# Kernel tuning notes

Hardware: AMD Instinct MI355X
Metric: run time of the kernel (lower is better)

## Reference

```python
import jax, jax.numpy as jnp
import numpy as np

DIM = 1024
EPS = 1e-5

def layer_norm(x, gamma, beta):
    mu = jnp.mean(x, axis=-1, keepdims=True)
    var = jnp.mean(jnp.square(x - mu), axis=-1, keepdims=True)
    return (x - mu) * jax.lax.rsqrt(var + EPS) * gamma + beta

def setup_inputs() -> dict:
    key = jax.random.key(0)
    k1, k2 = jax.random.split(key)
    B, Nv, Nt = 8, 4096, 4096
    visual_tokens = jax.random.normal(k1, (B, Nv, DIM), dtype=jnp.float32)
    text_tokens = jax.random.normal(k2, (B, Nt, DIM), dtype=jnp.float32)
    gamma_v = jnp.ones((DIM,), dtype=jnp.float32)
    beta_v = jnp.zeros((DIM,), dtype=jnp.float32)
    gamma_t = jnp.ones((DIM,), dtype=jnp.float32)
    beta_t = jnp.zeros((DIM,), dtype=jnp.float32)
    return {"visual_tokens": visual_tokens, "text_tokens": text_tokens,
            "gamma_v": gamma_v, "beta_v": beta_v,
            "gamma_t": gamma_t, "beta_t": beta_t}

def reference(visual_tokens, text_tokens, gamma_v, beta_v, gamma_t, beta_t):
    # Dual LayerNorm
    V = layer_norm(visual_tokens, gamma_v, beta_v)   # [B, Nv, D]
    T = layer_norm(text_tokens, gamma_t, beta_t)     # [B, Nt, D]
    scale = jnp.sqrt(jnp.asarray(DIM, dtype=V.dtype))  # note: sqrt(dim), per source
    scores = jnp.einsum('bvd,btd->bvt', V, T) / scale  # [B, Nv, Nt]
    attn = jax.nn.softmax(scores, axis=-1)
    out = jnp.einsum('bvt,btd->bvd', attn, T)          # [B, Nv, D]
    return out
```

## Files before the change

kernel.cpp:

```cpp
#include <hip/hip_runtime.h>
#include <hip/hip_bf16.h>
#include <stdint.h>

#define DIMD 1024
#define NSEQ 4096
#define BATCH 8
#define LN_EPS 1e-5f

typedef __attribute__((ext_vector_type(8))) short bf16x8;
typedef __attribute__((ext_vector_type(4))) float f32x4;
typedef __attribute__((ext_vector_type(4))) unsigned int u32x4;

__device__ __forceinline__ ushort f2bf(float f) {
  union { __hip_bfloat16 h; ushort u; } cv;
  cv.h = __float2bfloat16(f);
  return cv.u;
}

__device__ __forceinline__ float fexp2(float x) {
  return exp2f(x);
}

__device__ __forceinline__ void gload16(const void* g, void* l) {
  __builtin_amdgcn_global_load_lds(
      (const __attribute__((address_space(1))) uint32_t*)g,
      (__attribute__((address_space(3))) uint32_t*)l, 16, 0, 0);
}

#define MIDBAR()   asm volatile("s_barrier" ::: "memory")
#define ENDBAR()   asm volatile("s_waitcnt lgkmcnt(0)\n\ts_barrier" ::: "memory")
#define ENDBARV4() asm volatile("s_waitcnt vmcnt(4) lgkmcnt(0)\n\ts_barrier" ::: "memory")
#define ENDBARV0() asm volatile("s_waitcnt vmcnt(0) lgkmcnt(0)\n\ts_barrier" ::: "memory")

__device__ __forceinline__ int swz64(int byte) {
  return byte ^ (((byte >> 7) & 3) << 4);
}

__global__ __launch_bounds__(256) void ln_bf16_kernel(
    const float* __restrict__ x, const float* __restrict__ gamma,
    const float* __restrict__ beta, ushort* __restrict__ y, float scale)
{
  const int lane = threadIdx.x & 63;
  const int wv   = threadIdx.x >> 6;
  const size_t row = (size_t)blockIdx.x * 4 + wv;
  const float* xr = x + row * DIMD;

  float4 v[4];
#pragma unroll
  for (int c = 0; c < 4; ++c)
    v[c] = *(const float4*)(xr + c * 256 + lane * 4);

  float s = 0.f;
#pragma unroll
  for (int c = 0; c < 4; ++c) s += v[c].x + v[c].y + v[c].z + v[c].w;
#pragma unroll
  for (int m = 32; m >= 1; m >>= 1) s += __shfl_xor(s, m, 64);
  const float mean = s * (1.0f / DIMD);

  float vs = 0.f;
#pragma unroll
  for (int c = 0; c < 4; ++c) {
    float a0 = v[c].x - mean, a1 = v[c].y - mean;
    float a2 = v[c].z - mean, a3 = v[c].w - mean;
    vs += a0 * a0 + a1 * a1 + a2 * a2 + a3 * a3;
  }
#pragma unroll
  for (int m = 32; m >= 1; m >>= 1) vs += __shfl_xor(vs, m, 64);
  const float rstd = rsqrtf(vs * (1.0f / DIMD) + LN_EPS);

  ushort* yr = y + row * DIMD;
#pragma unroll
  for (int c = 0; c < 4; ++c) {
    const int d = c * 256 + lane * 4;
    float4 g  = *(const float4*)(gamma + d);
    float4 bb = *(const float4*)(beta + d);
    ushort4 o;
    o.x = f2bf(((v[c].x - mean) * rstd * g.x + bb.x) * scale);
    o.y = f2bf(((v[c].y - mean) * rstd * g.y + bb.y) * scale);
    o.z = f2bf(((v[c].z - mean) * rstd * g.z + bb.z) * scale);
    o.w = f2bf(((v[c].w - mean) * rstd * g.w + bb.w) * scale);
    *(ushort4*)(yr + d) = o;
  }
}

__global__ __launch_bounds__(256) void transpose_kernel(
    const ushort* __restrict__ src, ushort* __restrict__ dst)
{
  __shared__ ushort tile[64][72];
  const int t   = threadIdx.x;
  const int bid = blockIdx.x;
  const int b   = bid >> 10;
  const int rem = bid & 1023;
  const int n0  = (rem >> 4) << 6;
  const int d0  = (rem & 15) << 6;
  const ushort* sb = src + ((size_t)b * NSEQ) * DIMD;
  ushort* db       = dst + ((size_t)b * DIMD) * NSEQ;

#pragma unroll
  for (int k = 0; k < 2; ++k) {
    int c = t + 256 * k;
    int r = c >> 3, scol = (c & 7) * 8;
    *(uint4*)&tile[r][scol] =
        *(const uint4*)(sb + (size_t)(n0 + r) * DIMD + d0 + scol);
  }
  __syncthreads();
#pragma unroll
  for (int k = 0; k < 2; ++k) {
    int c = t + 256 * k;
    int dr = c >> 3, ns = (c & 7) * 8;
    union { ushort u[8]; uint4 q; } tv;
#pragma unroll
    for (int i = 0; i < 8; ++i) tv.u[i] = tile[ns + i][dr];
    *(uint4*)(db + (size_t)(d0 + dr) * NSEQ + n0 + ns) = tv.q;
  }
}

__device__ __forceinline__ void stage_chunk(const ushort* __restrict__ g,
                                            int ld, char* l, int tid) {
  const int o0 = tid * 16;
  const int o1 = o0 + 8192;
  const int s0 = swz64(o0);
  const int s1 = swz64(o1);
  gload16(g + (size_t)(s0 >> 6) * ld + ((s0 & 63) >> 1), l + o0);
  gload16(g + (size_t)(s1 >> 6) * ld + ((s1 & 63) >> 1), l + o1);
}

__device__ __forceinline__ void stage_lin(const ushort* __restrict__ g,
                                          char* l, int tid) {
  gload16(g + tid * 8,        l + tid * 16);
  gload16(g + 4096 + tid * 8, l + tid * 16 + 8192);
}

__device__ __forceinline__ bf16x8 ldsw_read(const char* base, int row, int lg) {
  return *(const bf16x8*)(base + swz64(row * 64 + lg * 16));
}

__device__ __forceinline__ void read_af(const char* Ac, int wm, int mh,
                                        int l15, int lg, bf16x8 (&af)[4]) {
#pragma unroll
  for (int m = 0; m < 4; ++m)
    af[m] = ldsw_read(Ac, wm * 128 + (mh * 4 + m) * 16 + l15, lg);
}
__device__ __forceinline__ void read_bf(const char* Bc, int wn,
                                        int l15, int lg, bf16x8 (&bf)[4]) {
#pragma unroll
  for (int n = 0; n < 4; ++n)
    bf[n] = ldsw_read(Bc, wn * 64 + n * 16 + l15, lg);
}

#define MFMA16(BASE)                                                          \
  do {                                                                        \
    MIDBAR();                                                                 \
    __builtin_amdgcn_s_setprio(1);                                            \
    _Pragma("unroll")                                                         \
    for (int m = 0; m < 4; ++m)                                               \
      _Pragma("unroll")                                                       \
      for (int n = 0; n < 4; ++n)                                             \
        acc[(BASE) + m][n] = __builtin_amdgcn_mfma_f32_16x16x32_bf16(         \
            af[m], bf[n], acc[(BASE) + m][n], 0, 0, 0);                       \
    __builtin_amdgcn_s_setprio(0);                                            \
  } while (0)

template <bool LINB>
__device__ __forceinline__ void gemm_core_A(
    const ushort* __restrict__ Ab, const ushort* __restrict__ Bb,
    int lda, int ldb, int NT, char* smem, f32x4 (&acc)[8][4],
    int tid, int wm, int wn, int l15, int lg)
{
  stage_chunk(Ab, lda, smem + 0, tid);
  if (LINB) stage_lin(Bb, smem + 32768, tid);
  else      stage_chunk(Bb, ldb, smem + 32768, tid);
  stage_chunk(Ab + 32, lda, smem + 16384, tid);
  if (LINB) stage_lin(Bb + 8192, smem + 49152, tid);
  else      stage_chunk(Bb + 32, ldb, smem + 49152, tid);
  ENDBARV4();

  for (int kt = 0; kt < NT; ++kt) {
    char* cb = smem + (kt & 1) * 65536;
    char* nbuf = smem + (((kt & 1) ^ 1) * 65536);
    const ushort* An = Ab + (size_t)(kt + 1) * 64;
    const ushort* Bn = LINB ? (Bb + (size_t)(kt + 1) * 16384)
                            : (Bb + (size_t)(kt + 1) * 64);
    const bool pf = (kt + 1 < NT);
    bf16x8 af[4], bf[4];

    read_af(cb + 0, wm, 0, l15, lg, af);
    read_bf(cb + 32768, wn, l15, lg, bf);
    if (pf) stage_chunk(An, lda, nbuf + 0, tid);
    MFMA16(0);
    ENDBAR();

    read_af(cb + 0, wm, 1, l15, lg, af);
    if (pf) {
      if (LINB) stage_lin(Bn, nbuf + 32768, tid);
      else      stage_chunk(Bn, ldb, nbuf + 32768, tid);
    }
    MFMA16(4);
    if (pf) { ENDBARV4(); } else { ENDBARV0(); }

    read_af(cb + 16384, wm, 0, l15, lg, af);
    read_bf(cb + 49152, wn, l15, lg, bf);
    if (pf) stage_chunk(An + 32, lda, nbuf + 16384, tid);
    MFMA16(0);
    ENDBAR();

    read_af(cb + 16384, wm, 1, l15, lg, af);
    if (pf) {
      if (LINB) stage_lin(Bn + 8192, nbuf + 49152, tid);
      else      stage_chunk(Bn + 32, ldb, nbuf + 49152, tid);
    }
    MFMA16(4);
    if (pf) { ENDBARV4(); } else { ENDBAR(); }
  }
}

__global__ __launch_bounds__(512, 2) void gemm1_256(
    const ushort* __restrict__ Q, const ushort* __restrict__ K,
    ushort* __restrict__ S, float* __restrict__ Rsum,
    int b0, size_t s_stride)
{
  extern __shared__ char smem[];
  const int tid  = threadIdx.x;
  const int lane = tid & 63;
  const int wave = tid >> 6;
  const int wm = wave >> 2, wn = wave & 3;
  const int l15 = lane & 15, lg = lane >> 4;

  int by, bxx, bzc;
  if (gridDim.x == 8 * 64) {
    const int hw = blockIdx.x;
    bzc = hw & 7;
    const int inner = hw >> 3;
    bxx = inner & 3;
    by  = inner >> 2;
  } else {
    by = blockIdx.y; bxx = blockIdx.x; bzc = 0;
  }

  const int bz   = b0 + bzc;
  const int row0 = by * 256;
  const ushort* Qb = Q + (size_t)bz * NSEQ * DIMD + (size_t)row0 * DIMD;
  const ushort* Kb0 = K + (size_t)bz * NSEQ * DIMD;

  float vsum[4] = {0.f, 0.f, 0.f, 0.f};

#pragma unroll 1
  for (int st = 0; st < 4; ++st) {
    const int bx = bxx * 4 + st;
    const ushort* Kb = Kb0 + (size_t)(bx * 256) * DIMD;

    f32x4 acc[8][4];
#pragma unroll
    for (int m = 0; m < 8; ++m)
#pragma unroll
      for (int n = 0; n < 4; ++n) acc[m][n] = 0.0f;

    gemm_core_A<false>(Kb, Qb, DIMD, DIMD, DIMD / 64, smem, acc,
                       tid, wm, wn, l15, lg);

#pragma unroll
    for (int ti = 0; ti < 8; ++ti) {
      const int tl   = wm * 128 + ti * 16 + lg * 4;
      const int ktl  = tl >> 6;
      const int half = (tl >> 5) & 1;
      const int tcol = tl & 31;
      char* img = smem + (ktl * 2 + half) * 16384;
#pragma unroll
      for (int vi = 0; vi < 4; ++vi) {
        const int vrow = wn * 64 + vi * 16 + l15;
        float p0 = fexp2(acc[ti][vi][0]);
        float p1 = fexp2(acc[ti][vi][1]);
        float p2 = fexp2(acc[ti][vi][2]);
        float p3 = fexp2(acc[ti][vi][3]);
        vsum[vi] += (p0 + p1) + (p2 + p3);
        unsigned long long pk =
            (unsigned long long)f2bf(p0)        |
            ((unsigned long long)f2bf(p1) << 16) |
            ((unsigned long long)f2bf(p2) << 32) |
            ((unsigned long long)f2bf(p3) << 48);
        *(unsigned long long*)(img + swz64(vrow * 64 + tcol * 2)) = pk;
      }
    }
    __syncthreads();

    ushort* region = S + (size_t)bzc * s_stride
                   + (size_t)by * 1048576 + (size_t)bx * 65536;
#pragma unroll
    for (int j = 0; j < 16; ++j) {
      const int off = (j * 512 + tid) * 16;
      u32x4 vle = *(const u32x4*)(smem + off);
      __builtin_nontemporal_store(vle, (u32x4*)((char*)region + off));
    }
    __syncthreads();
  }

  float* Rs = Rsum + (size_t)bz * NSEQ;
#pragma unroll
  for (int vi = 0; vi < 4; ++vi) {
    float s = vsum[vi];
    s += __shfl_xor(s, 16, 64);
    s += __shfl_xor(s, 32, 64);
    if (lg == 0)
      atomicAdd(Rs + row0 + wn * 64 + vi * 16 + l15, s);
  }
}

__global__ __launch_bounds__(512, 2) void gemm2_256(
    const ushort* __restrict__ S, const ushort* __restrict__ Kt,
    const float* __restrict__ Rsum, float* __restrict__ Out,
    int b0, size_t s_stride)
{
  extern __shared__ char smem[];
  const int tid  = threadIdx.x;
  const int lane = tid & 63;
  const int wave = tid >> 6;
  const int wm = wave >> 2, wn = wave & 3;
  const int l15 = lane & 15, lg = lane >> 4;

  int bx, by, bzc;
  if (gridDim.z == BATCH) {
    const int hw = blockIdx.x + (blockIdx.y << 2) + (blockIdx.z << 6);
    bzc = hw & 7;
    const int inner = hw >> 3;
    bx = inner & 3; by = inner >> 2;
  } else {
    bx = blockIdx.x; by = blockIdx.y; bzc = 0;
  }

  const int bz   = b0 + bzc;
  const int row0 = by * 256;
  const int col0 = bx * 256;
  const ushort* Sbase = S + (size_t)bzc * s_stride + (size_t)by * 1048576;
  const ushort* Vtb = Kt + ((size_t)bz * DIMD + col0) * NSEQ;

  f32x4 acc[8][4];
#pragma unroll
  for (int m = 0; m < 8; ++m)
#pragma unroll
    for (int n = 0; n < 4; ++n) acc[m][n] = 0.0f;

  gemm_core_A<true>(Vtb, Sbase, NSEQ, 0, NSEQ / 64, smem, acc, tid, wm, wn, l15, lg);

  const float* Rs = Rsum + (size_t)bz * NSEQ;
  float* Ob = Out + (size_t)bz * NSEQ * DIMD;
  float inv[4];
#pragma unroll
  for (int vi = 0; vi < 4; ++vi)
    inv[vi] = 1.0f / Rs[row0 + wn * 64 + vi * 16 + l15];
#pragma unroll
  for (int di = 0; di < 8; ++di) {
#pragma unroll
    for (int vi = 0; vi < 4; ++vi) {
      const int v = row0 + wn * 64 + vi * 16 + l15;
      const int d = col0 + wm * 128 + di * 16 + lg * 4;
      f32x4 o = acc[di][vi] * inv[vi];
      *(f32x4*)(Ob + (size_t)v * DIMD + d) = o;
    }
  }
}

extern "C" void kernel_launch(void* const* d_in, const int* in_sizes, int n_in,
                              void* d_out, int out_size, void* d_ws, size_t ws_size,
                              hipStream_t stream) {
  const float* vis = (const float*)d_in[0];
  const float* txt = (const float*)d_in[1];
  const float* gv  = (const float*)d_in[2];
  const float* bv  = (const float*)d_in[3];
  const float* gt  = (const float*)d_in[4];
  const float* bt  = (const float*)d_in[5];
  float* out = (float*)d_out;

  const size_t tokens = (size_t)BATCH * NSEQ * DIMD;
  ushort* Qbf = (ushort*)d_ws;
  ushort* Kbf = Qbf + tokens;
  ushort* Ktb = Kbf + tokens;
  char*   wsb = (char*)d_ws;
  float*  Rsum = (float*)(wsb + 201326592);
  ushort* Sbuf = (ushort*)(wsb + 201457664);

  const size_t S_FULL = (size_t)BATCH * NSEQ * NSEQ * 2;
  const size_t NEED_FULL = 201457664 + S_FULL;

  ln_bf16_kernel<<<BATCH * NSEQ / 4, 256, 0, stream>>>(vis, gv, bv, Qbf,
                                                       0.045084219f);
  ln_bf16_kernel<<<BATCH * NSEQ / 4, 256, 0, stream>>>(txt, gt, bt, Kbf, 1.0f);
  transpose_kernel<<<BATCH * (NSEQ / 64) * (DIMD / 64), 256, 0, stream>>>(Kbf, Ktb);

  (void)hipFuncSetAttribute((const void*)gemm1_256,
                      hipFuncAttributeMaxDynamicSharedMemorySize, 131072);
  (void)hipFuncSetAttribute((const void*)gemm2_256,
                      hipFuncAttributeMaxDynamicSharedMemorySize, 131072);

  (void)hipMemsetAsync(Rsum, 0, (size_t)BATCH * NSEQ * sizeof(float), stream);

  if (ws_size >= NEED_FULL) {
    gemm1_256<<<dim3(8 * 64, 1, 1), 512, 131072, stream>>>(
        Qbf, Kbf, Sbuf, Rsum, 0, (size_t)NSEQ * NSEQ);
    gemm2_256<<<dim3(4, 16, BATCH), 512, 131072, stream>>>(
        Sbuf, Ktb, Rsum, out, 0, (size_t)NSEQ * NSEQ);
  } else {
    for (int b = 0; b < BATCH; ++b) {
      gemm1_256<<<dim3(4, 16, 1), 512, 131072, stream>>>(
          Qbf, Kbf, Sbuf, Rsum, b, 0);
      gemm2_256<<<dim3(4, 16, 1), 512, 131072, stream>>>(
          Sbuf, Ktb, Rsum, out, b, 0);
    }
  }
}
```

Baseline: 616.8 us.

## Flatten score GEMM into one pipelined K loop across column tiles, store P directly

Merges the four per-tile GEMM calls into a single 64-step double-buffered loop, so loads for the next column tile are prefetched while the current one finishes and no pipeline drain or refill happens between tiles. The exp2 and bf16 pack results are now written straight to global memory in the swizzled layout, replacing the LDS staging and the nontemporal copy-out along with its two block barriers. The costs are scattered 8-byte global stores in place of coalesced 16-byte nontemporal ones, and the softmax epilogue now runs inside the main loop.

```diff
diff --git a/kernel.cpp b/kernel.cpp
--- a/kernel.cpp
+++ b/kernel.cpp
@@ -9,7 +9,6 @@
 
 typedef __attribute__((ext_vector_type(8))) short bf16x8;
 typedef __attribute__((ext_vector_type(4))) float f32x4;
-typedef __attribute__((ext_vector_type(4))) unsigned int u32x4;
 
 __device__ __forceinline__ ushort f2bf(float f) {
   union { __hip_bfloat16 h; ushort u; } cv;
@@ -239,59 +238,87 @@
 
   const int bz   = b0 + bzc;
   const int row0 = by * 256;
-  const ushort* Qb = Q + (size_t)bz * NSEQ * DIMD + (size_t)row0 * DIMD;
-  const ushort* Kb0 = K + (size_t)bz * NSEQ * DIMD;
-
+  const ushort* Qb  = Q + (size_t)bz * NSEQ * DIMD + (size_t)row0 * DIMD;
+  const ushort* Kb0 = K + (size_t)bz * NSEQ * DIMD
+                    + (size_t)(bxx * 4) * 256 * DIMD;
+  char* Sreg = (char*)(S + (size_t)bzc * s_stride + (size_t)by * 1048576)
+             + (size_t)bxx * 4 * 131072;
+
+  f32x4 acc[8][4];
+#pragma unroll
+  for (int m = 0; m < 8; ++m)
+#pragma unroll
+    for (int n = 0; n < 4; ++n) acc[m][n] = 0.0f;
   float vsum[4] = {0.f, 0.f, 0.f, 0.f};
 
+  stage_chunk(Kb0,      DIMD, smem + 0,     tid);
+  stage_chunk(Qb,       DIMD, smem + 32768, tid);
+  stage_chunk(Kb0 + 32, DIMD, smem + 16384, tid);
+  stage_chunk(Qb + 32,  DIMD, smem + 49152, tid);
+  ENDBARV4();
+
 #pragma unroll 1
-  for (int st = 0; st < 4; ++st) {
-    const int bx = bxx * 4 + st;
-    const ushort* Kb = Kb0 + (size_t)(bx * 256) * DIMD;
-
-    f32x4 acc[8][4];
-#pragma unroll
-    for (int m = 0; m < 8; ++m)
-#pragma unroll
-      for (int n = 0; n < 4; ++n) acc[m][n] = 0.0f;
-
-    gemm_core_A<false>(Kb, Qb, DIMD, DIMD, DIMD / 64, smem, acc,
-                       tid, wm, wn, l15, lg);
-
-#pragma unroll
-    for (int ti = 0; ti < 8; ++ti) {
-      const int tl   = wm * 128 + ti * 16 + lg * 4;
-      const int ktl  = tl >> 6;
-      const int half = (tl >> 5) & 1;
-      const int tcol = tl & 31;
-      char* img = smem + (ktl * 2 + half) * 16384;
-#pragma unroll
-      for (int vi = 0; vi < 4; ++vi) {
-        const int vrow = wn * 64 + vi * 16 + l15;
-        float p0 = fexp2(acc[ti][vi][0]);
-        float p1 = fexp2(acc[ti][vi][1]);
-        float p2 = fexp2(acc[ti][vi][2]);
-        float p3 = fexp2(acc[ti][vi][3]);
-        vsum[vi] += (p0 + p1) + (p2 + p3);
-        unsigned long long pk =
-            (unsigned long long)f2bf(p0)        |
-            ((unsigned long long)f2bf(p1) << 16) |
-            ((unsigned long long)f2bf(p2) << 32) |
-            ((unsigned long long)f2bf(p3) << 48);
-        *(unsigned long long*)(img + swz64(vrow * 64 + tcol * 2)) = pk;
+  for (int kt = 0; kt < 64; ++kt) {
+    char* cb   = smem + (kt & 1) * 65536;
+    char* nbuf = smem + (((kt & 1) ^ 1) * 65536);
+    const int vn = kt + 1;
+    const bool pf = (vn < 64);
+    const ushort* An = Kb0 + (size_t)(vn >> 4) * 256 * DIMD + (vn & 15) * 64;
+    const ushort* Bn = Qb + (vn & 15) * 64;
+    bf16x8 af[4], bf[4];
+
+    read_af(cb + 0, wm, 0, l15, lg, af);
+    read_bf(cb + 32768, wn, l15, lg, bf);
+    if (pf) stage_chunk(An, DIMD, nbuf + 0, tid);
+    MFMA16(0);
+    ENDBAR();
+
+    read_af(cb + 0, wm, 1, l15, lg, af);
+    if (pf) stage_chunk(Bn, DIMD, nbuf + 32768, tid);
+    MFMA16(4);
+    if (pf) { ENDBARV4(); } else { ENDBARV0(); }
+
+    read_af(cb + 16384, wm, 0, l15, lg, af);
+    read_bf(cb + 49152, wn, l15, lg, bf);
+    if (pf) stage_chunk(An + 32, DIMD, nbuf + 16384, tid);
+    MFMA16(0);
+    ENDBAR();
+
+    read_af(cb + 16384, wm, 1, l15, lg, af);
+    if (pf) stage_chunk(Bn + 32, DIMD, nbuf + 49152, tid);
+    MFMA16(4);
+    if (pf) { ENDBARV4(); } else { ENDBAR(); }
+
+    if ((kt & 15) == 15) {
+      char* region = Sreg + (size_t)(kt >> 4) * 131072;
+#pragma unroll
+      for (int ti = 0; ti < 8; ++ti) {
+        const int tl   = wm * 128 + ti * 16 + lg * 4;
+        const int ktl  = tl >> 6;
+        const int half = (tl >> 5) & 1;
+        const int tcol = tl & 31;
+        char* img = region + (ktl * 2 + half) * 16384;
+#pragma unroll
+        for (int vi = 0; vi < 4; ++vi) {
+          const int vrow = wn * 64 + vi * 16 + l15;
+          float p0 = fexp2(acc[ti][vi][0]);
+          float p1 = fexp2(acc[ti][vi][1]);
+          float p2 = fexp2(acc[ti][vi][2]);
+          float p3 = fexp2(acc[ti][vi][3]);
+          vsum[vi] += (p0 + p1) + (p2 + p3);
+          unsigned long long pk =
+              (unsigned long long)f2bf(p0)        |
+              ((unsigned long long)f2bf(p1) << 16) |
+              ((unsigned long long)f2bf(p2) << 32) |
+              ((unsigned long long)f2bf(p3) << 48);
+          *(unsigned long long*)(img + swz64(vrow * 64 + tcol * 2)) = pk;
+        }
       }
+#pragma unroll
+      for (int m = 0; m < 8; ++m)
+#pragma unroll
+        for (int n = 0; n < 4; ++n) acc[m][n] = 0.0f;
     }
-    __syncthreads();
-
-    ushort* region = S + (size_t)bzc * s_stride
-                   + (size_t)by * 1048576 + (size_t)bx * 65536;
-#pragma unroll
-    for (int j = 0; j < 16; ++j) {
-      const int off = (j * 512 + tid) * 16;
-      u32x4 vle = *(const u32x4*)(smem + off);
-      __builtin_nontemporal_store(vle, (u32x4*)((char*)region + off));
-    }
-    __syncthreads();
   }
 
   float* Rs = Rsum + (size_t)bz * NSEQ;
```

New measurement: 620.1 us. No clear change (+0.5%).
